# Performance work log

Measured on AMD Instinct MI355X. Metric: run time of the kernel, lower is better.

Reference implementation:

```python
import jax, jax.numpy as jnp
import numpy as np

L = 10
DIM = 4
TABLE = 1 << 16
BASE_RES = 16.0
PLS = 2.0
HID = 64
SCALE_MULTI = 0.5
DENSITY_OFFSET = -1.0
SCENE_SCALING = 2.0
PRIMES = (np.uint32(1), np.uint32(2654435761), np.uint32(805459861))


def _safe_exp(x):
    return jnp.exp(jnp.clip(x, -30.0, 10.0))


def _l2norm(x, eps=1e-8):
    return x / jnp.sqrt(jnp.sum(x * x, -1, keepdims=True) + eps)


def _circumcenters(tets):
    # tets: [T,4,3]; solve 2(vi-v0).c = |vi|^2-|v0|^2
    v0 = tets[:, 0]
    A = 2.0 * (tets[:, 1:] - v0[:, None, :]) + 1e-6 * jnp.eye(3, dtype=tets.dtype)
    b = jnp.sum(tets[:, 1:] ** 2, -1) - jnp.sum(v0 ** 2, -1)[:, None]
    c = jnp.linalg.solve(A, b[..., None])[..., 0]
    r = jnp.linalg.norm(c - v0, axis=-1)
    return c, r


def _project_to_tet(p, tets):
    # clamp-and-renormalize barycentric coordinates (approximate projection)
    v0 = tets[:, 0]
    E = tets[:, 1:] - v0[:, None, :]
    M = jnp.einsum('tid,tjd->tij', E, E) + 1e-6 * jnp.eye(3, dtype=tets.dtype)
    rhs = jnp.einsum('tid,td->ti', E, p - v0)
    lam = jnp.linalg.solve(M, rhs[..., None])[..., 0]
    bary = jnp.concatenate([1.0 - lam.sum(-1, keepdims=True), lam], -1)
    bary = jnp.clip(bary, 0.0, 1.0)
    bary = bary / jnp.clip(bary.sum(-1, keepdims=True), 1e-6, None)
    return jnp.einsum('tv,tvd->td', bary, tets)


def _contract_mean_std(x, std):
    # mipnerf-360 style scene contraction of mean; std scaled by |J| ~ 1/n^2
    n = jnp.maximum(jnp.linalg.norm(x, axis=-1, keepdims=True), 1e-9)
    cx = jnp.where(n <= 1.0, x, (2.0 - 1.0 / n) * x / n)
    cs = std * jnp.where(n[..., 0] <= 1.0, 1.0, 1.0 / (n[..., 0] ** 2))
    return cx, cs


def _hash_encode(pos, tables):
    # pos [T,3] in [0,1); tables [L, TABLE, DIM]; multiresolution hash grid
    mask = np.uint32(TABLE - 1)
    pos = jnp.clip(pos, 0.0, 1.0 - 1e-6)
    feats = []
    for l in range(L):
        res = float(np.floor(BASE_RES * (PLS ** l)))
        x = pos * res
        f = jnp.floor(x)
        w = x - f
        fi = f.astype(jnp.uint32)
        acc = jnp.zeros(pos.shape[:-1] + (DIM,), pos.dtype)
        for cz in (0, 1):
            for cy in (0, 1):
                for cx in (0, 1):
                    c = fi + jnp.asarray((cx, cy, cz), jnp.uint32)
                    h = ((c[..., 0] * PRIMES[0]) ^ (c[..., 1] * PRIMES[1]) ^ (c[..., 2] * PRIMES[2])) & mask
                    wt = ((w[..., 0] if cx else 1.0 - w[..., 0]) *
                          (w[..., 1] if cy else 1.0 - w[..., 1]) *
                          (w[..., 2] if cz else 1.0 - w[..., 2]))
                    acc = acc + tables[l][h.astype(jnp.int32)] * wt[..., None]
        feats.append(acc)
    return jnp.stack(feats, axis=1)  # [T, L, DIM]


def _forward(vertices, indices, center, tables, W1, b1, W2, b2, W3, b3):
    tets = vertices[indices]  # [T,4,3] gather
    cc, radius = _circumcenters(tets)
    cc = _project_to_tet(cc, tets)
    normalized = (cc - center) / SCENE_SCALING
    cv, cr = _contract_mean_std(normalized, radius / SCENE_SCALING)
    cr = cr * SCALE_MULTI
    n = jnp.arange(L, dtype=vertices.dtype)
    erf_x = 1.0 / jnp.sqrt(PLS * 4.0 * n[None, :] * cr[:, None] + 1e-12)
    scaling = jax.lax.erf(erf_x)  # [T, L] per-level erf anti-aliasing scale
    pos = cv * 0.25 + 0.5  # contracted [-2,2] -> [0,1]
    feats = _hash_encode(pos, tables) * scaling[..., None]
    h = feats.reshape(feats.shape[0], L * DIM)
    h = jax.nn.selu(h @ W1 + b1)
    h = jax.nn.selu(h @ W2 + b2)
    out = h @ W3 + b3  # [T, 13]
    density = _safe_exp(out[:, 0] + DENSITY_OFFSET)
    pairs = ((0, 1), (0, 2), (0, 3), (1, 2), (1, 3), (2, 3))
    el = jnp.stack([jnp.linalg.norm(tets[:, i] - tets[:, j], axis=1) for i, j in pairs], 0).max(0)
    alpha = 1.0 - jnp.exp(-density * el)
    V = vertices.shape[0]
    vertex_alpha = jnp.zeros((V,), vertices.dtype).at[indices].max(
        jnp.broadcast_to(alpha[:, None], indices.shape))  # scatter amax
    fs = out[:, 1:]
    base = fs[:, :3] + 0.5
    grads = jnp.clip(base[:, :, None], 0.0, None) * jnp.tanh(fs[:, 3:12].reshape(-1, 3, 3))
    offs = _l2norm(tets - cc[:, None, :])
    vcol = base[:, None, :] + jnp.einsum('tcd,tvd->tvc', grads, offs)  # [T,4,3]
    return vertex_alpha, vcol


def setup_inputs() -> dict:
    key = jax.random.key(0)
    ks = jax.random.split(key, 8)
    V, T = 100000, 500000
    vertices = jax.random.normal(ks[0], (V, 3), jnp.float32) * 0.5
    indices = jax.random.randint(ks[1], (T, 4), 0, V, jnp.int32)
    center = jnp.zeros((1, 3), jnp.float32)
    tables = jax.random.normal(ks[2], (L, TABLE, DIM), jnp.float32) * 1e-2
    def lin(k, i, o):
        s = (6.0 / (i + o)) ** 0.5
        return jax.random.uniform(k, (i, o), jnp.float32, -s, s)
    return dict(vertices=vertices, indices=indices, center=center, tables=tables,
                W1=lin(ks[3], L * DIM, HID), b1=jnp.zeros((HID,), jnp.float32),
                W2=lin(ks[4], HID, HID), b2=jnp.zeros((HID,), jnp.float32),
                W3=lin(ks[5], HID, 13), b3=jnp.zeros((13,), jnp.float32))


def reference(vertices, indices, center, tables, W1, b1, W2, b2, W3, b3):
    return _forward(vertices, indices, center, tables, W1, b1, W2, b2, W3, b3)
```

## Files before the change

### kernel.cpp

```cpp
#include <hip/hip_runtime.h>
#include <math.h>

#define NLVL 10
#define TBL 65536
#define NHID 64
#define NIN 40
#define LDP 68

typedef __attribute__((ext_vector_type(8))) short bf16x8;
typedef __attribute__((ext_vector_type(4))) float f32x4;
typedef unsigned int uint;
typedef unsigned short ushort;

__device__ __forceinline__ float selu_f(float x) {
    return 1.0507009873554805f * (x > 0.0f ? x : 1.6732632423543772f * (__expf(x) - 1.0f));
}
__device__ __forceinline__ float fast_tanh(float x) {
    float xx = fminf(fmaxf(x, -15.0f), 15.0f);
    float t = __expf(2.0f * xx);
    return (t - 1.0f) / (t + 1.0f);
}
__device__ __forceinline__ short2 tsplit(float x) {
    uint u = __float_as_uint(x);
    short hi = (short)(u >> 16);
    float hif = __uint_as_float(u & 0xFFFF0000u);
    float lo = x - hif;
    short los = (short)(__float_as_uint(lo) >> 16);
    short2 s; s.x = hi; s.y = los;
    return s;
}

__device__ __forceinline__ void solve3d(const double A[3][3], const double b[3], double x[3]) {
    double a00=A[0][0], a01=A[0][1], a02=A[0][2];
    double a10=A[1][0], a11=A[1][1], a12=A[1][2];
    double a20=A[2][0], a21=A[2][1], a22=A[2][2];
    double C00 =  (a11*a22 - a12*a21);
    double C01 = -(a10*a22 - a12*a20);
    double C02 =  (a10*a21 - a11*a20);
    double C10 = -(a01*a22 - a02*a21);
    double C11 =  (a00*a22 - a02*a20);
    double C12 = -(a00*a21 - a01*a20);
    double C20 =  (a01*a12 - a02*a11);
    double C21 = -(a00*a12 - a02*a10);
    double C22 =  (a00*a11 - a01*a10);
    double det = a00*C00 + a01*C01 + a02*C02;
    double inv = 1.0 / det;
    x[0] = (C00*b[0] + C10*b[1] + C20*b[2]) * inv;
    x[1] = (C01*b[0] + C11*b[1] + C21*b[2]) * inv;
    x[2] = (C02*b[0] + C12*b[1] + C22*b[2]) * inv;
}

__global__ void __launch_bounds__(256) zero_alpha_kernel(float* out, int V) {
    int i = blockIdx.x * blockDim.x + threadIdx.x;
    if (i < V) out[i] = 0.0f;
}

__device__ __forceinline__ void enc2(const float4* __restrict__ tb4,
                                     float px, float py, float pz, float crf,
                                     int l0, float f[8]) {
    uint idx[2][8];
    float wt[2][8];
    #pragma unroll
    for (int h = 0; h < 2; ++h) {
        int l = l0 + h;
        float res = (float)(16 << l);
        float x0 = px*res, x1 = py*res, x2 = pz*res;
        float f0 = floorf(x0), f1 = floorf(x1), f2 = floorf(x2);
        float w0 = x0-f0, w1 = x1-f1, w2 = x2-f2;
        uint i0 = (uint)f0, i1 = (uint)f1, i2 = (uint)f2;
        #pragma unroll
        for (int cn = 0; cn < 8; ++cn) {
            uint cx = (uint)(cn & 1), cy = (uint)((cn >> 1) & 1), cz = (uint)((cn >> 2) & 1);
            idx[h][cn] = (((i0 + cx) * 1u) ^ ((i1 + cy) * 2654435761u) ^ ((i2 + cz) * 805459861u)) & 65535u;
            wt[h][cn] = (cx ? w0 : 1.0f - w0) * (cy ? w1 : 1.0f - w1) * (cz ? w2 : 1.0f - w2);
        }
    }
    float4 v[2][8];
    #pragma unroll
    for (int h = 0; h < 2; ++h)
        #pragma unroll
        for (int cn = 0; cn < 8; ++cn)
            v[h][cn] = tb4[(size_t)(l0+h)*TBL + idx[h][cn]];
    #pragma unroll
    for (int h = 0; h < 2; ++h) {
        float a0=0.f, a1=0.f, a2=0.f, a3=0.f;
        #pragma unroll
        for (int cn = 0; cn < 8; ++cn) {
            float w = wt[h][cn];
            a0 = fmaf(v[h][cn].x, w, a0);
            a1 = fmaf(v[h][cn].y, w, a1);
            a2 = fmaf(v[h][cn].z, w, a2);
            a3 = fmaf(v[h][cn].w, w, a3);
        }
        float sc = erff(rsqrtf(8.0f*(float)(l0+h)*crf + 1e-12f));
        f[h*4+0] = a0*sc; f[h*4+1] = a1*sc; f[h*4+2] = a2*sc; f[h*4+3] = a3*sc;
    }
}

__device__ __forceinline__ void store_split8(const float f[8],
                                             ushort* __restrict__ fh,
                                             ushort* __restrict__ fl) {
    bf16x8 h8, l8;
    #pragma unroll
    for (int j = 0; j < 8; ++j) {
        short2 sp = tsplit(f[j]);
        h8[j] = sp.x; l8[j] = sp.y;
    }
    *reinterpret_cast<bf16x8*>(fh) = h8;
    *reinterpret_cast<bf16x8*>(fl) = l8;
}

__global__ void __launch_bounds__(256) geom01_kernel(
    const float* __restrict__ vertices,
    const int*   __restrict__ indices,
    const float* __restrict__ center,
    const float* __restrict__ tables,
    float* __restrict__ aux,
    ushort* __restrict__ feats_hi,
    ushort* __restrict__ feats_lo, int T)
{
    int t = blockIdx.x * blockDim.x + threadIdx.x;
    if (t >= T) return;

    double p[4][3];
    #pragma unroll
    for (int v = 0; v < 4; ++v) {
        int vid = indices[t*4+v];
        p[v][0] = (double)vertices[vid*3+0];
        p[v][1] = (double)vertices[vid*3+1];
        p[v][2] = (double)vertices[vid*3+2];
    }

    double A[3][3], bb[3];
    double v0sq = p[0][0]*p[0][0] + p[0][1]*p[0][1] + p[0][2]*p[0][2];
    #pragma unroll
    for (int i = 0; i < 3; ++i) {
        #pragma unroll
        for (int j = 0; j < 3; ++j)
            A[i][j] = 2.0*(p[i+1][j] - p[0][j]) + (i==j ? 1e-6 : 0.0);
        bb[i] = p[i+1][0]*p[i+1][0] + p[i+1][1]*p[i+1][1] + p[i+1][2]*p[i+1][2] - v0sq;
    }
    double c[3];
    solve3d(A, bb, c);
    double dx0 = c[0]-p[0][0], dy0 = c[1]-p[0][1], dz0 = c[2]-p[0][2];
    double radius = sqrt(dx0*dx0 + dy0*dy0 + dz0*dz0);

    double E[3][3];
    #pragma unroll
    for (int i = 0; i < 3; ++i)
        #pragma unroll
        for (int j = 0; j < 3; ++j)
            E[i][j] = p[i+1][j] - p[0][j];
    double M[3][3], rhs[3];
    #pragma unroll
    for (int i = 0; i < 3; ++i) {
        #pragma unroll
        for (int k = 0; k < 3; ++k)
            M[i][k] = E[i][0]*E[k][0] + E[i][1]*E[k][1] + E[i][2]*E[k][2] + (i==k ? 1e-6 : 0.0);
        rhs[i] = E[i][0]*dx0 + E[i][1]*dy0 + E[i][2]*dz0;
    }
    double lam[3];
    solve3d(M, rhs, lam);
    double bary[4];
    bary[0] = 1.0 - lam[0] - lam[1] - lam[2];
    bary[1] = lam[0]; bary[2] = lam[1]; bary[3] = lam[2];
    double bs = 0.0;
    #pragma unroll
    for (int v = 0; v < 4; ++v) {
        bary[v] = fmin(fmax(bary[v], 0.0), 1.0);
        bs += bary[v];
    }
    bs = fmax(bs, 1e-6);
    double cc[3];
    #pragma unroll
    for (int j = 0; j < 3; ++j)
        cc[j] = (bary[0]*p[0][j] + bary[1]*p[1][j] + bary[2]*p[2][j] + bary[3]*p[3][j]) / bs;

    double xv[3];
    xv[0] = (cc[0] - (double)center[0]) * 0.5;
    xv[1] = (cc[1] - (double)center[1]) * 0.5;
    xv[2] = (cc[2] - (double)center[2]) * 0.5;
    double nrm = sqrt(xv[0]*xv[0] + xv[1]*xv[1] + xv[2]*xv[2]);
    double n = fmax(nrm, 1e-9);
    double cv[3], cs;
    if (n <= 1.0) {
        cv[0]=xv[0]; cv[1]=xv[1]; cv[2]=xv[2];
        cs = radius * 0.5;
    } else {
        double f = (2.0 - 1.0/n) / n;
        cv[0]=xv[0]*f; cv[1]=xv[1]*f; cv[2]=xv[2]*f;
        cs = radius * 0.5 / (n*n);
    }
    float crf = (float)(cs * 0.5);

    float px = fminf(fmaxf((float)(cv[0]*0.25 + 0.5), 0.0f), 1.0f - 1e-6f);
    float py = fminf(fmaxf((float)(cv[1]*0.25 + 0.5), 0.0f), 1.0f - 1e-6f);
    float pz = fminf(fmaxf((float)(cv[2]*0.25 + 0.5), 0.0f), 1.0f - 1e-6f);

    float el = 0.0f;
    #pragma unroll
    for (int a = 0; a < 3; ++a)
        #pragma unroll
        for (int bq = a+1; bq < 4; ++bq) {
            float ddx = (float)(p[a][0]-p[bq][0]);
            float ddy = (float)(p[a][1]-p[bq][1]);
            float ddz = (float)(p[a][2]-p[bq][2]);
            el = fmaxf(el, sqrtf(ddx*ddx + ddy*ddy + ddz*ddz));
        }

    size_t st = (size_t)T;
    aux[0*st + t] = px;
    aux[1*st + t] = py;
    aux[2*st + t] = pz;
    aux[3*st + t] = crf;
    aux[4*st + t] = (float)cc[0];
    aux[5*st + t] = (float)cc[1];
    aux[6*st + t] = (float)cc[2];
    aux[7*st + t] = el;

    const float4* tb4 = reinterpret_cast<const float4*>(tables);
    float f01[8];
    enc2(tb4, px, py, pz, crf, 0, f01);
    store_split8(f01, feats_hi + (size_t)t*NIN, feats_lo + (size_t)t*NIN);
}

template<int L0>
__global__ void __launch_bounds__(256) hash_pass_kernel(
    const float* __restrict__ tables,
    const float* __restrict__ aux,
    ushort* __restrict__ feats_hi,
    ushort* __restrict__ feats_lo, int T)
{
    int t = blockIdx.x * blockDim.x + threadIdx.x;
    if (t >= T) return;
    size_t st = (size_t)T;
    float px = aux[0*st + t];
    float py = aux[1*st + t];
    float pz = aux[2*st + t];
    float crf = aux[3*st + t];
    const float4* tb4 = reinterpret_cast<const float4*>(tables);

    float f[8];
    enc2(tb4, px, py, pz, crf, L0, f);
    store_split8(f, feats_hi + (size_t)t*NIN + L0*4, feats_lo + (size_t)t*NIN + L0*4);
}

__global__ void __launch_bounds__(256, 2) mlp_mfma_kernel(
    const ushort* __restrict__ feats_hi,
    const ushort* __restrict__ feats_lo,
    const float* __restrict__ aux,
    const float* __restrict__ vertices,
    const int*   __restrict__ indices,
    const float* __restrict__ W1, const float* __restrict__ b1,
    const float* __restrict__ W2, const float* __restrict__ b2,
    const float* __restrict__ W3, const float* __restrict__ b3,
    float* __restrict__ out, int T, int V)
{
    __shared__ __align__(16) float hts[4][16][LDP];

    const int tid  = threadIdx.x;
    const int wid  = tid >> 6;
    const int lane = tid & 63;
    const int r    = lane & 15;
    const int g    = lane >> 4;

    bf16x8 w1h[2][4];
    bf16x8 w1l0[4];
    #pragma unroll
    for (int s = 0; s < 2; ++s)
        #pragma unroll
        for (int nt = 0; nt < 4; ++nt) {
            bf16x8 h, lo;
            #pragma unroll
            for (int j = 0; j < 8; ++j) {
                int k = s*32 + g*8 + j;
                float w = (k < NIN) ? W1[k*NHID + nt*16 + r] : 0.0f;
                short2 sp = tsplit(w);
                h[j] = sp.x; lo[j] = sp.y;
            }
            w1h[s][nt] = h;
            if (s == 0) w1l0[nt] = lo;
        }
    bf16x8 w2h[2][4], w2l[2][4];
    #pragma unroll
    for (int s = 0; s < 2; ++s)
        #pragma unroll
        for (int nt = 0; nt < 4; ++nt) {
            bf16x8 h, lo;
            #pragma unroll
            for (int j = 0; j < 8; ++j) {
                int k = s*32 + g*8 + j;
                float w = W2[k*NHID + nt*16 + r];
                short2 sp = tsplit(w);
                h[j] = sp.x; lo[j] = sp.y;
            }
            w2h[s][nt] = h; w2l[s][nt] = lo;
        }
    bf16x8 w3h[2], w3l[2];
    #pragma unroll
    for (int s = 0; s < 2; ++s) {
        bf16x8 h, lo;
        #pragma unroll
        for (int j = 0; j < 8; ++j) {
            int k = s*32 + g*8 + j;
            float w = (r < 13) ? W3[k*13 + r] : 0.0f;
            short2 sp = tsplit(w);
            h[j] = sp.x; lo[j] = sp.y;
        }
        w3h[s] = h; w3l[s] = lo;
    }
    float b1v[4], b2v[4];
    #pragma unroll
    for (int nt = 0; nt < 4; ++nt) { b1v[nt] = b1[nt*16 + r]; b2v[nt] = b2[nt*16 + r]; }
    float b3v = (r < 13) ? b3[r] : 0.0f;

    const size_t st = (size_t)T;
    const int nmt = (T + 15) >> 4;
    const int gw = blockIdx.x * 4 + wid;
    const int gstride = gridDim.x * 4;
    const bf16x8 zfrag = {0,0,0,0,0,0,0,0};

    if (gw >= nmt) return;

    bf16x8 ah0, al0, ah1;
    {
        int trow = gw*16 + r;
        bool rowok = trow < T;
        const ushort* fh = feats_hi + (size_t)trow * NIN;
        const ushort* fl = feats_lo + (size_t)trow * NIN;
        ah0 = rowok ? *reinterpret_cast<const bf16x8*>(fh + g*8) : zfrag;
        al0 = rowok ? *reinterpret_cast<const bf16x8*>(fl + g*8) : zfrag;
        ah1 = (rowok && g == 0) ? *reinterpret_cast<const bf16x8*>(fh + 32) : zfrag;
    }

    for (int mt = gw; mt < nmt; mt += gstride) {
        const int t0 = mt * 16;

        const int te = t0 + (lane >> 2);
        const int ev = lane & 3;
        const bool teok = te < T;
        int vid = teok ? indices[te*4 + ev] : 0;
        float el  = teok ? aux[7*st + te] : 0.0f;
        float cc0 = teok ? aux[4*st + te] : 0.0f;
        float cc1 = teok ? aux[5*st + te] : 0.0f;
        float cc2 = teok ? aux[6*st + te] : 0.0f;

        __builtin_amdgcn_s_setprio(1);
        #pragma unroll
        for (int nt = 0; nt < 4; ++nt) {
            f32x4 acc = {0.f, 0.f, 0.f, 0.f};
            acc = __builtin_amdgcn_mfma_f32_16x16x32_bf16(ah0, w1h[0][nt], acc, 0, 0, 0);
            acc = __builtin_amdgcn_mfma_f32_16x16x32_bf16(ah0, w1l0[nt],  acc, 0, 0, 0);
            acc = __builtin_amdgcn_mfma_f32_16x16x32_bf16(al0, w1h[0][nt], acc, 0, 0, 0);
            acc = __builtin_amdgcn_mfma_f32_16x16x32_bf16(ah1, w1h[1][nt], acc, 0, 0, 0);
            #pragma unroll
            for (int q = 0; q < 4; ++q)
                hts[wid][g*4 + q][nt*16 + r] = selu_f(acc[q] + b1v[nt]);
        }
        __builtin_amdgcn_s_setprio(0);

        const int mtn = mt + gstride;
        bf16x8 nah0 = zfrag, nal0 = zfrag, nah1 = zfrag;
        if (mtn < nmt) {
            int trow = mtn*16 + r;
            bool rowok = trow < T;
            const ushort* fh = feats_hi + (size_t)trow * NIN;
            const ushort* fl = feats_lo + (size_t)trow * NIN;
            if (rowok) {
                nah0 = *reinterpret_cast<const bf16x8*>(fh + g*8);
                nal0 = *reinterpret_cast<const bf16x8*>(fl + g*8);
                if (g == 0) nah1 = *reinterpret_cast<const bf16x8*>(fh + 32);
            }
        }

        float pvx = vertices[vid*3+0];
        float pvy = vertices[vid*3+1];
        float pvz = vertices[vid*3+2];

        asm volatile("s_waitcnt lgkmcnt(0)" ::: "memory");

        bf16x8 a2h[2], a2l[2];
        #pragma unroll
        for (int s = 0; s < 2; ++s) {
            float4 u0 = *reinterpret_cast<const float4*>(&hts[wid][r][s*32 + g*8]);
            float4 u1 = *reinterpret_cast<const float4*>(&hts[wid][r][s*32 + g*8 + 4]);
            bf16x8 h, lo;
            short2 sp;
            sp = tsplit(u0.x); h[0]=sp.x; lo[0]=sp.y;
            sp = tsplit(u0.y); h[1]=sp.x; lo[1]=sp.y;
            sp = tsplit(u0.z); h[2]=sp.x; lo[2]=sp.y;
            sp = tsplit(u0.w); h[3]=sp.x; lo[3]=sp.y;
            sp = tsplit(u1.x); h[4]=sp.x; lo[4]=sp.y;
            sp = tsplit(u1.y); h[5]=sp.x; lo[5]=sp.y;
            sp = tsplit(u1.z); h[6]=sp.x; lo[6]=sp.y;
            sp = tsplit(u1.w); h[7]=sp.x; lo[7]=sp.y;
            a2h[s] = h; a2l[s] = lo;
        }
        asm volatile("s_waitcnt lgkmcnt(0)" ::: "memory");
        float h2v[4][4];
        __builtin_amdgcn_s_setprio(1);
        #pragma unroll
        for (int nt = 0; nt < 4; ++nt) {
            f32x4 acc = {0.f, 0.f, 0.f, 0.f};
            #pragma unroll
            for (int s = 0; s < 2; ++s) {
                acc = __builtin_amdgcn_mfma_f32_16x16x32_bf16(a2h[s], w2h[s][nt], acc, 0, 0, 0);
                acc = __builtin_amdgcn_mfma_f32_16x16x32_bf16(a2h[s], w2l[s][nt], acc, 0, 0, 0);
                acc = __builtin_amdgcn_mfma_f32_16x16x32_bf16(a2l[s], w2h[s][nt], acc, 0, 0, 0);
            }
            #pragma unroll
            for (int q = 0; q < 4; ++q) h2v[nt][q] = selu_f(acc[q] + b2v[nt]);
        }
        __builtin_amdgcn_s_setprio(0);
        #pragma unroll
        for (int nt = 0; nt < 4; ++nt)
            #pragma unroll
            for (int q = 0; q < 4; ++q)
                hts[wid][g*4 + q][nt*16 + r] = h2v[nt][q];
        asm volatile("s_waitcnt lgkmcnt(0)" ::: "memory");

        bf16x8 a3h[2], a3l[2];
        #pragma unroll
        for (int s = 0; s < 2; ++s) {
            float4 u0 = *reinterpret_cast<const float4*>(&hts[wid][r][s*32 + g*8]);
            float4 u1 = *reinterpret_cast<const float4*>(&hts[wid][r][s*32 + g*8 + 4]);
            bf16x8 h, lo;
            short2 sp;
            sp = tsplit(u0.x); h[0]=sp.x; lo[0]=sp.y;
            sp = tsplit(u0.y); h[1]=sp.x; lo[1]=sp.y;
            sp = tsplit(u0.z); h[2]=sp.x; lo[2]=sp.y;
            sp = tsplit(u0.w); h[3]=sp.x; lo[3]=sp.y;
            sp = tsplit(u1.x); h[4]=sp.x; lo[4]=sp.y;
            sp = tsplit(u1.y); h[5]=sp.x; lo[5]=sp.y;
            sp = tsplit(u1.z); h[6]=sp.x; lo[6]=sp.y;
            sp = tsplit(u1.w); h[7]=sp.x; lo[7]=sp.y;
            a3h[s] = h; a3l[s] = lo;
        }
        asm volatile("s_waitcnt lgkmcnt(0)" ::: "memory");
        {
            f32x4 acc = {0.f, 0.f, 0.f, 0.f};
            __builtin_amdgcn_s_setprio(1);
            #pragma unroll
            for (int s = 0; s < 2; ++s) {
                acc = __builtin_amdgcn_mfma_f32_16x16x32_bf16(a3h[s], w3h[s], acc, 0, 0, 0);
                acc = __builtin_amdgcn_mfma_f32_16x16x32_bf16(a3h[s], w3l[s], acc, 0, 0, 0);
                acc = __builtin_amdgcn_mfma_f32_16x16x32_bf16(a3l[s], w3h[s], acc, 0, 0, 0);
            }
            __builtin_amdgcn_s_setprio(0);
            #pragma unroll
            for (int q = 0; q < 4; ++q)
                hts[wid][g*4 + q][r] = acc[q] + b3v;
        }
        asm volatile("s_waitcnt lgkmcnt(0)" ::: "memory");

        if (teok) {
            const float* orow = hts[wid][lane >> 2];
            float4 o0 = *reinterpret_cast<const float4*>(&orow[0]);
            float4 o1 = *reinterpret_cast<const float4*>(&orow[4]);
            float4 o2 = *reinterpret_cast<const float4*>(&orow[8]);
            float o12 = orow[12];

            float dv = fminf(fmaxf(o0.x - 1.0f, -30.0f), 10.0f);
            float density = __expf(dv);
            float alpha = 1.0f - __expf(-density * el);
            int ab = __float_as_int(alpha);
            atomicMax((int*)out + vid, ab);

            float base0 = o0.y + 0.5f, base1 = o0.z + 0.5f, base2 = o0.w + 0.5f;
            float bc0 = fmaxf(base0, 0.0f), bc1 = fmaxf(base1, 0.0f), bc2 = fmaxf(base2, 0.0f);
            float g00 = bc0*fast_tanh(o1.x), g01 = bc0*fast_tanh(o1.y), g02 = bc0*fast_tanh(o1.z);
            float g10 = bc1*fast_tanh(o1.w), g11 = bc1*fast_tanh(o2.x), g12 = bc1*fast_tanh(o2.y);
            float g20 = bc2*fast_tanh(o2.z), g21 = bc2*fast_tanh(o2.w), g22 = bc2*fast_tanh(o12);

            float ox = pvx-cc0, oy = pvy-cc1, oz = pvz-cc2;
            float inv = rsqrtf(ox*ox + oy*oy + oz*oz + 1e-8f);
            float q0 = ox*inv, q1 = oy*inv, q2 = oz*inv;
            float* vout = out + V + (size_t)te * 12 + ev*3;
            vout[0] = base0 + g00*q0 + g01*q1 + g02*q2;
            vout[1] = base1 + g10*q0 + g11*q1 + g12*q2;
            vout[2] = base2 + g20*q0 + g21*q1 + g22*q2;
        }
        asm volatile("s_waitcnt lgkmcnt(0)" ::: "memory");

        ah0 = nah0; al0 = nal0; ah1 = nah1;
    }
}

__global__ void __launch_bounds__(256) tet_forward_fused(
    const float* __restrict__ vertices,
    const int*   __restrict__ indices,
    const float* __restrict__ center,
    const float* __restrict__ tables,
    const float* __restrict__ W1, const float* __restrict__ b1,
    const float* __restrict__ W2, const float* __restrict__ b2,
    const float* __restrict__ W3, const float* __restrict__ b3,
    float* __restrict__ out, int T, int V)
{
    int t = blockIdx.x * blockDim.x + threadIdx.x;
    if (t >= T) return;

    double p[4][3];
    int vv[4];
    #pragma unroll
    for (int v = 0; v < 4; ++v) {
        vv[v] = indices[t*4+v];
        p[v][0] = (double)vertices[vv[v]*3+0];
        p[v][1] = (double)vertices[vv[v]*3+1];
        p[v][2] = (double)vertices[vv[v]*3+2];
    }
    double A[3][3], bb[3];
    double v0sq = p[0][0]*p[0][0] + p[0][1]*p[0][1] + p[0][2]*p[0][2];
    #pragma unroll
    for (int i = 0; i < 3; ++i) {
        #pragma unroll
        for (int j = 0; j < 3; ++j)
            A[i][j] = 2.0*(p[i+1][j] - p[0][j]) + (i==j ? 1e-6 : 0.0);
        bb[i] = p[i+1][0]*p[i+1][0] + p[i+1][1]*p[i+1][1] + p[i+1][2]*p[i+1][2] - v0sq;
    }
    double c[3];
    solve3d(A, bb, c);
    double dx0 = c[0]-p[0][0], dy0 = c[1]-p[0][1], dz0 = c[2]-p[0][2];
    double radius = sqrt(dx0*dx0 + dy0*dy0 + dz0*dz0);
    double E[3][3];
    #pragma unroll
    for (int i = 0; i < 3; ++i)
        #pragma unroll
        for (int j = 0; j < 3; ++j)
            E[i][j] = p[i+1][j] - p[0][j];
    double M[3][3], rhs[3];
    #pragma unroll
    for (int i = 0; i < 3; ++i) {
        #pragma unroll
        for (int k = 0; k < 3; ++k)
            M[i][k] = E[i][0]*E[k][0] + E[i][1]*E[k][1] + E[i][2]*E[k][2] + (i==k ? 1e-6 : 0.0);
        rhs[i] = E[i][0]*dx0 + E[i][1]*dy0 + E[i][2]*dz0;
    }
    double lam[3];
    solve3d(M, rhs, lam);
    double bary[4];
    bary[0] = 1.0 - lam[0] - lam[1] - lam[2];
    bary[1] = lam[0]; bary[2] = lam[1]; bary[3] = lam[2];
    double bs = 0.0;
    #pragma unroll
    for (int v = 0; v < 4; ++v) { bary[v] = fmin(fmax(bary[v], 0.0), 1.0); bs += bary[v]; }
    bs = fmax(bs, 1e-6);
    double cc[3];
    #pragma unroll
    for (int j = 0; j < 3; ++j)
        cc[j] = (bary[0]*p[0][j] + bary[1]*p[1][j] + bary[2]*p[2][j] + bary[3]*p[3][j]) / bs;
    double xv[3];
    xv[0] = (cc[0] - (double)center[0]) * 0.5;
    xv[1] = (cc[1] - (double)center[1]) * 0.5;
    xv[2] = (cc[2] - (double)center[2]) * 0.5;
    double nrm = sqrt(xv[0]*xv[0] + xv[1]*xv[1] + xv[2]*xv[2]);
    double n = fmax(nrm, 1e-9);
    double cv[3], cs;
    if (n <= 1.0) { cv[0]=xv[0]; cv[1]=xv[1]; cv[2]=xv[2]; cs = radius * 0.5; }
    else { double f = (2.0 - 1.0/n) / n; cv[0]=xv[0]*f; cv[1]=xv[1]*f; cv[2]=xv[2]*f; cs = radius * 0.5 / (n*n); }
    float crf = (float)(cs * 0.5);
    float pos0 = fminf(fmaxf((float)(cv[0]*0.25 + 0.5), 0.0f), 1.0f - 1e-6f);
    float pos1 = fminf(fmaxf((float)(cv[1]*0.25 + 0.5), 0.0f), 1.0f - 1e-6f);
    float pos2 = fminf(fmaxf((float)(cv[2]*0.25 + 0.5), 0.0f), 1.0f - 1e-6f);

    float h0[NIN];
    float res = 16.0f;
    #pragma unroll
    for (int l = 0; l < NLVL; ++l) {
        float x0 = pos0*res, x1 = pos1*res, x2 = pos2*res;
        float f0 = floorf(x0), f1 = floorf(x1), f2 = floorf(x2);
        float w0 = x0-f0, w1 = x1-f1, w2 = x2-f2;
        unsigned i0 = (unsigned)f0, i1 = (unsigned)f1, i2 = (unsigned)f2;
        float a0=0.f, a1=0.f, a2=0.f, a3=0.f;
        #pragma unroll
        for (int cn = 0; cn < 8; ++cn) {
            unsigned cx = (unsigned)(cn & 1), cy = (unsigned)((cn >> 1) & 1), cz = (unsigned)((cn >> 2) & 1);
            unsigned hh = ((i0 + cx) * 1u) ^ ((i1 + cy) * 2654435761u) ^ ((i2 + cz) * 805459861u);
            hh &= 65535u;
            float wt = (cx ? w0 : 1.0f - w0) * (cy ? w1 : 1.0f - w1) * (cz ? w2 : 1.0f - w2);
            const float4 tv = *reinterpret_cast<const float4*>(tables + ((size_t)l*TBL + hh)*4);
            a0 = fmaf(tv.x, wt, a0); a1 = fmaf(tv.y, wt, a1);
            a2 = fmaf(tv.z, wt, a2); a3 = fmaf(tv.w, wt, a3);
        }
        float sc = erff(rsqrtf(8.0f*(float)l*crf + 1e-12f));
        h0[l*4+0] = a0*sc; h0[l*4+1] = a1*sc; h0[l*4+2] = a2*sc; h0[l*4+3] = a3*sc;
        res *= 2.0f;
    }

    float h1[NHID];
    #pragma unroll
    for (int j = 0; j < NHID; ++j) h1[j] = b1[j];
    #pragma unroll
    for (int i = 0; i < NIN; ++i) {
        float hi = h0[i];
        #pragma unroll
        for (int j = 0; j < NHID; ++j) h1[j] = fmaf(hi, W1[i*NHID + j], h1[j]);
    }
    #pragma unroll
    for (int j = 0; j < NHID; ++j) h1[j] = selu_f(h1[j]);

    float o[13];
    #pragma unroll
    for (int k = 0; k < 13; ++k) o[k] = b3[k];
    #pragma unroll
    for (int half = 0; half < 2; ++half) {
        float h2h[32];
        #pragma unroll
        for (int jj = 0; jj < 32; ++jj) h2h[jj] = b2[half*32 + jj];
        #pragma unroll
        for (int i = 0; i < NHID; ++i) {
            float hi = h1[i];
            #pragma unroll
            for (int jj = 0; jj < 32; ++jj)
                h2h[jj] = fmaf(hi, W2[i*NHID + half*32 + jj], h2h[jj]);
        }
        #pragma unroll
        for (int jj = 0; jj < 32; ++jj) {
            float hv = selu_f(h2h[jj]);
            #pragma unroll
            for (int k = 0; k < 13; ++k)
                o[k] = fmaf(hv, W3[(half*32 + jj)*13 + k], o[k]);
        }
    }

    float dv = fminf(fmaxf(o[0] - 1.0f, -30.0f), 10.0f);
    float density = __expf(dv);
    float el = 0.0f;
    #pragma unroll
    for (int a = 0; a < 3; ++a)
        #pragma unroll
        for (int bq = a+1; bq < 4; ++bq) {
            float ddx = (float)(p[a][0]-p[bq][0]);
            float ddy = (float)(p[a][1]-p[bq][1]);
            float ddz = (float)(p[a][2]-p[bq][2]);
            el = fmaxf(el, sqrtf(ddx*ddx + ddy*ddy + ddz*ddz));
        }
    float alpha = 1.0f - __expf(-density * el);
    int ab = __float_as_int(alpha);
    atomicMax((int*)out + vv[0], ab);
    atomicMax((int*)out + vv[1], ab);
    atomicMax((int*)out + vv[2], ab);
    atomicMax((int*)out + vv[3], ab);

    float base0 = o[1] + 0.5f, base1 = o[2] + 0.5f, base2 = o[3] + 0.5f;
    float bc0 = fmaxf(base0, 0.0f), bc1 = fmaxf(base1, 0.0f), bc2 = fmaxf(base2, 0.0f);
    float g00 = bc0*fast_tanh(o[4]),  g01 = bc0*fast_tanh(o[5]),  g02 = bc0*fast_tanh(o[6]);
    float g10 = bc1*fast_tanh(o[7]),  g11 = bc1*fast_tanh(o[8]),  g12 = bc1*fast_tanh(o[9]);
    float g20 = bc2*fast_tanh(o[10]), g21 = bc2*fast_tanh(o[11]), g22 = bc2*fast_tanh(o[12]);

    float* vout = out + V + (size_t)t * 12;
    #pragma unroll
    for (int v = 0; v < 4; ++v) {
        float ox = (float)(p[v][0]-cc[0]), oy = (float)(p[v][1]-cc[1]), oz = (float)(p[v][2]-cc[2]);
        float inv = rsqrtf(ox*ox + oy*oy + oz*oz + 1e-8f);
        float q0 = ox*inv, q1 = oy*inv, q2 = oz*inv;
        vout[v*3+0] = base0 + g00*q0 + g01*q1 + g02*q2;
        vout[v*3+1] = base1 + g10*q0 + g11*q1 + g12*q2;
        vout[v*3+2] = base2 + g20*q0 + g21*q1 + g22*q2;
    }
}

extern "C" void kernel_launch(void* const* d_in, const int* in_sizes, int n_in,
                              void* d_out, int out_size, void* d_ws, size_t ws_size,
                              hipStream_t stream) {
    const float* vertices = (const float*)d_in[0];
    const int*   indices  = (const int*)d_in[1];
    const float* center   = (const float*)d_in[2];
    const float* tables   = (const float*)d_in[3];
    const float* W1 = (const float*)d_in[4];
    const float* b1 = (const float*)d_in[5];
    const float* W2 = (const float*)d_in[6];
    const float* b2 = (const float*)d_in[7];
    const float* W3 = (const float*)d_in[8];
    const float* b3 = (const float*)d_in[9];
    int V = in_sizes[0] / 3;
    int T = in_sizes[1] / 4;
    float* out = (float*)d_out;

    hipLaunchKernelGGL(zero_alpha_kernel, dim3((V + 255) / 256), dim3(256), 0, stream, out, V);

    size_t need = (size_t)T * 48 * sizeof(float);
    dim3 grid((T + 255) / 256), blk(256);
    if (ws_size >= need) {
        float* aux = (float*)d_ws;
        ushort* feats_hi = (ushort*)(aux + (size_t)T * 8);
        ushort* feats_lo = feats_hi + (size_t)T * NIN;
        hipLaunchKernelGGL(geom01_kernel, grid, blk, 0, stream,
                           vertices, indices, center, tables, aux, feats_hi, feats_lo, T);
        hipLaunchKernelGGL((hash_pass_kernel<2>), grid, blk, 0, stream, tables, aux, feats_hi, feats_lo, T);
        hipLaunchKernelGGL((hash_pass_kernel<4>), grid, blk, 0, stream, tables, aux, feats_hi, feats_lo, T);
        hipLaunchKernelGGL((hash_pass_kernel<6>), grid, blk, 0, stream, tables, aux, feats_hi, feats_lo, T);
        hipLaunchKernelGGL((hash_pass_kernel<8>), grid, blk, 0, stream, tables, aux, feats_hi, feats_lo, T);
        hipLaunchKernelGGL(mlp_mfma_kernel, dim3(1024), blk, 0, stream, feats_hi, feats_lo, aux,
                           vertices, indices, W1, b1, W2, b2, W3, b3, out, T, V);
    } else {
        hipLaunchKernelGGL(tet_forward_fused, grid, blk, 0, stream,
                           vertices, indices, center, tables, W1, b1, W2, b2, W3, b3, out, T, V);
    }
}
```

Measured before the change: 237.3 us.

## Stage split MLP weights in LDS to free registers and raise occupancy

Moves the bf16 hi/lo split weight fragments for all three MLP layers out of per-thread registers into shared memory, filled cooperatively by the block once. MFMA B operands are then read from LDS each tile. The launch bound goes from 2 to 3 blocks per SM and the grid shrinks from 1024 to 768 blocks to match. This trades register pressure for extra LDS reads per tile and more LDS per block, which may contend with the existing hts traffic.

```diff
diff --git a/kernel.cpp b/kernel.cpp
--- a/kernel.cpp
+++ b/kernel.cpp
@@ -245,7 +245,7 @@
     store_split8(f, feats_hi + (size_t)t*NIN + L0*4, feats_lo + (size_t)t*NIN + L0*4);
 }
 
-__global__ void __launch_bounds__(256, 2) mlp_mfma_kernel(
+__global__ void __launch_bounds__(256, 3) mlp_mfma_kernel(
     const ushort* __restrict__ feats_hi,
     const ushort* __restrict__ feats_lo,
     const float* __restrict__ aux,
@@ -257,6 +257,12 @@
     float* __restrict__ out, int T, int V)
 {
     __shared__ __align__(16) float hts[4][16][LDP];
+    __shared__ bf16x8 sW1h[8*64];
+    __shared__ bf16x8 sW1l[4*64];
+    __shared__ bf16x8 sW2h[8*64];
+    __shared__ bf16x8 sW2l[8*64];
+    __shared__ bf16x8 sW3h[2*64];
+    __shared__ bf16x8 sW3l[2*64];
 
     const int tid  = threadIdx.x;
     const int wid  = tid >> 6;
@@ -264,51 +270,52 @@
     const int r    = lane & 15;
     const int g    = lane >> 4;
 
-    bf16x8 w1h[2][4];
-    bf16x8 w1l0[4];
-    #pragma unroll
-    for (int s = 0; s < 2; ++s)
-        #pragma unroll
-        for (int nt = 0; nt < 4; ++nt) {
-            bf16x8 h, lo;
-            #pragma unroll
-            for (int j = 0; j < 8; ++j) {
-                int k = s*32 + g*8 + j;
-                float w = (k < NIN) ? W1[k*NHID + nt*16 + r] : 0.0f;
-                short2 sp = tsplit(w);
-                h[j] = sp.x; lo[j] = sp.y;
-            }
-            w1h[s][nt] = h;
-            if (s == 0) w1l0[nt] = lo;
-        }
-    bf16x8 w2h[2][4], w2l[2][4];
-    #pragma unroll
-    for (int s = 0; s < 2; ++s)
-        #pragma unroll
-        for (int nt = 0; nt < 4; ++nt) {
-            bf16x8 h, lo;
-            #pragma unroll
-            for (int j = 0; j < 8; ++j) {
-                int k = s*32 + g*8 + j;
-                float w = W2[k*NHID + nt*16 + r];
-                short2 sp = tsplit(w);
-                h[j] = sp.x; lo[j] = sp.y;
-            }
-            w2h[s][nt] = h; w2l[s][nt] = lo;
-        }
-    bf16x8 w3h[2], w3l[2];
-    #pragma unroll
-    for (int s = 0; s < 2; ++s) {
+    for (int slot = tid; slot < 8*64; slot += 256) {
+        int set = slot >> 6, l = slot & 63;
+        int s = set >> 2, nt = set & 3;
+        int rr = l & 15, gg = l >> 4;
         bf16x8 h, lo;
         #pragma unroll
         for (int j = 0; j < 8; ++j) {
-            int k = s*32 + g*8 + j;
-            float w = (r < 13) ? W3[k*13 + r] : 0.0f;
+            int k = s*32 + gg*8 + j;
+            float w = (k < NIN) ? W1[k*NHID + nt*16 + rr] : 0.0f;
             short2 sp = tsplit(w);
             h[j] = sp.x; lo[j] = sp.y;
         }
-        w3h[s] = h; w3l[s] = lo;
-    }
+        sW1h[slot] = h;
+        if (s == 0) sW1l[nt*64 + l] = lo;
+    }
+    for (int slot = tid; slot < 8*64; slot += 256) {
+        int set = slot >> 6, l = slot & 63;
+        int s = set >> 2, nt = set & 3;
+        int rr = l & 15, gg = l >> 4;
+        bf16x8 h, lo;
+        #pragma unroll
+        for (int j = 0; j < 8; ++j) {
+            int k = s*32 + gg*8 + j;
+            float w = W2[k*NHID + nt*16 + rr];
+            short2 sp = tsplit(w);
+            h[j] = sp.x; lo[j] = sp.y;
+        }
+        sW2h[slot] = h;
+        sW2l[slot] = lo;
+    }
+    for (int slot = tid; slot < 2*64; slot += 256) {
+        int s = slot >> 6, l = slot & 63;
+        int rr = l & 15, gg = l >> 4;
+        bf16x8 h, lo;
+        #pragma unroll
+        for (int j = 0; j < 8; ++j) {
+            int k = s*32 + gg*8 + j;
+            float w = (rr < 13) ? W3[k*13 + rr] : 0.0f;
+            short2 sp = tsplit(w);
+            h[j] = sp.x; lo[j] = sp.y;
+        }
+        sW3h[slot] = h;
+        sW3l[slot] = lo;
+    }
+    __syncthreads();
+
     float b1v[4], b2v[4];
     #pragma unroll
     for (int nt = 0; nt < 4; ++nt) { b1v[nt] = b1[nt*16 + r]; b2v[nt] = b2[nt*16 + r]; }
@@ -349,10 +356,10 @@
         #pragma unroll
         for (int nt = 0; nt < 4; ++nt) {
             f32x4 acc = {0.f, 0.f, 0.f, 0.f};
-            acc = __builtin_amdgcn_mfma_f32_16x16x32_bf16(ah0, w1h[0][nt], acc, 0, 0, 0);
-            acc = __builtin_amdgcn_mfma_f32_16x16x32_bf16(ah0, w1l0[nt],  acc, 0, 0, 0);
-            acc = __builtin_amdgcn_mfma_f32_16x16x32_bf16(al0, w1h[0][nt], acc, 0, 0, 0);
-            acc = __builtin_amdgcn_mfma_f32_16x16x32_bf16(ah1, w1h[1][nt], acc, 0, 0, 0);
+            acc = __builtin_amdgcn_mfma_f32_16x16x32_bf16(ah0, sW1h[nt*64 + lane],       acc, 0, 0, 0);
+            acc = __builtin_amdgcn_mfma_f32_16x16x32_bf16(ah0, sW1l[nt*64 + lane],       acc, 0, 0, 0);
+            acc = __builtin_amdgcn_mfma_f32_16x16x32_bf16(al0, sW1h[nt*64 + lane],       acc, 0, 0, 0);
+            acc = __builtin_amdgcn_mfma_f32_16x16x32_bf16(ah1, sW1h[(4+nt)*64 + lane],   acc, 0, 0, 0);
             #pragma unroll
             for (int q = 0; q < 4; ++q)
                 hts[wid][g*4 + q][nt*16 + r] = selu_f(acc[q] + b1v[nt]);
@@ -404,9 +411,9 @@
             f32x4 acc = {0.f, 0.f, 0.f, 0.f};
             #pragma unroll
             for (int s = 0; s < 2; ++s) {
-                acc = __builtin_amdgcn_mfma_f32_16x16x32_bf16(a2h[s], w2h[s][nt], acc, 0, 0, 0);
-                acc = __builtin_amdgcn_mfma_f32_16x16x32_bf16(a2h[s], w2l[s][nt], acc, 0, 0, 0);
-                acc = __builtin_amdgcn_mfma_f32_16x16x32_bf16(a2l[s], w2h[s][nt], acc, 0, 0, 0);
+                acc = __builtin_amdgcn_mfma_f32_16x16x32_bf16(a2h[s], sW2h[(s*4+nt)*64 + lane], acc, 0, 0, 0);
+                acc = __builtin_amdgcn_mfma_f32_16x16x32_bf16(a2h[s], sW2l[(s*4+nt)*64 + lane], acc, 0, 0, 0);
+                acc = __builtin_amdgcn_mfma_f32_16x16x32_bf16(a2l[s], sW2h[(s*4+nt)*64 + lane], acc, 0, 0, 0);
             }
             #pragma unroll
             for (int q = 0; q < 4; ++q) h2v[nt][q] = selu_f(acc[q] + b2v[nt]);
@@ -442,9 +449,9 @@
             __builtin_amdgcn_s_setprio(1);
             #pragma unroll
             for (int s = 0; s < 2; ++s) {
-                acc = __builtin_amdgcn_mfma_f32_16x16x32_bf16(a3h[s], w3h[s], acc, 0, 0, 0);
-                acc = __builtin_amdgcn_mfma_f32_16x16x32_bf16(a3h[s], w3l[s], acc, 0, 0, 0);
-                acc = __builtin_amdgcn_mfma_f32_16x16x32_bf16(a3l[s], w3h[s], acc, 0, 0, 0);
+                acc = __builtin_amdgcn_mfma_f32_16x16x32_bf16(a3h[s], sW3h[s*64 + lane], acc, 0, 0, 0);
+                acc = __builtin_amdgcn_mfma_f32_16x16x32_bf16(a3h[s], sW3l[s*64 + lane], acc, 0, 0, 0);
+                acc = __builtin_amdgcn_mfma_f32_16x16x32_bf16(a3l[s], sW3h[s*64 + lane], acc, 0, 0, 0);
             }
             __builtin_amdgcn_s_setprio(0);
             #pragma unroll
@@ -690,7 +697,7 @@
         hipLaunchKernelGGL((hash_pass_kernel<4>), grid, blk, 0, stream, tables, aux, feats_hi, feats_lo, T);
         hipLaunchKernelGGL((hash_pass_kernel<6>), grid, blk, 0, stream, tables, aux, feats_hi, feats_lo, T);
         hipLaunchKernelGGL((hash_pass_kernel<8>), grid, blk, 0, stream, tables, aux, feats_hi, feats_lo, T);
-        hipLaunchKernelGGL(mlp_mfma_kernel, dim3(1024), blk, 0, stream, feats_hi, feats_lo, aux,
+        hipLaunchKernelGGL(mlp_mfma_kernel, dim3(768), blk, 0, stream, feats_hi, feats_lo, aux,
                            vertices, indices, W1, b1, W2, b2, W3, b3, out, T, V);
     } else {
         hipLaunchKernelGGL(tet_forward_fused, grid, blk, 0, stream,
```

Measured after the change: 230.7 us. -2.8%, faster.
